# Performance work log

Hardware: AMD Instinct MI355X
Metric: run time of the kernel (lower is better)

Reference implementation:

```python
import jax, jax.numpy as jnp
import numpy as np

B, S, D, H, DH, L, FF = 1, 4096, 768, 12, 64, 12, 3072
V, P = 50265, 4098
BLK = 256          # block size for banded attention
W_ONE = 256        # one-sided window (attention_window=512)
EPS = 1e-5


def layernorm(x, g, b):
    mu = jnp.mean(x, axis=-1, keepdims=True)
    var = jnp.mean((x - mu) ** 2, axis=-1, keepdims=True)
    return (x - mu) * jax.lax.rsqrt(var + EPS) * g + b


def sliding_attn(q, k, v, mask):
    # q,k,v: [B,H,S,DH]; mask: [B,S] (1=keep). Band |i-j| <= W_ONE.
    nb = S // BLK
    scale = 1.0 / np.sqrt(DH)
    qb = (q * scale).reshape(B, H, nb, BLK, DH)
    kp = jnp.pad(k, ((0, 0), (0, 0), (BLK, BLK), (0, 0))).reshape(B, H, nb + 2, BLK, DH)
    vp = jnp.pad(v, ((0, 0), (0, 0), (BLK, BLK), (0, 0))).reshape(B, H, nb + 2, BLK, DH)
    # each query block attends to key blocks [b-1, b, b+1] -> 3*BLK keys
    kb = jnp.concatenate([kp[:, :, :-2], kp[:, :, 1:-1], kp[:, :, 2:]], axis=3)
    vb = jnp.concatenate([vp[:, :, :-2], vp[:, :, 1:-1], vp[:, :, 2:]], axis=3)
    scores = jnp.einsum('bhnqd,bhnkd->bhnqk', qb, kb)  # [B,H,nb,BLK,3BLK]
    p = jnp.arange(BLK)[:, None]
    o = jnp.arange(3 * BLK)[None, :]
    rel = o - BLK - p
    band = (rel >= -W_ONE) & (rel <= W_ONE)            # [BLK,3BLK]
    mp = jnp.pad(mask.astype(bool), ((0, 0), (BLK, BLK))).reshape(B, nb + 2, BLK)
    mb = jnp.concatenate([mp[:, :-2], mp[:, 1:-1], mp[:, 2:]], axis=2)  # [B,nb,3BLK]
    valid = band[None, None, None, :, :] & mb[:, None, :, None, :]
    scores = jnp.where(valid, scores, jnp.asarray(-1e9, scores.dtype))
    probs = jax.nn.softmax(scores, axis=-1)
    out = jnp.einsum('bhnqk,bhnkd->bhnqd', probs, vb)
    return out.reshape(B, H, S, DH)


def setup_inputs() -> dict:
    keys = iter(jax.random.split(jax.random.key(0), 64))
    rn = lambda shape, s=0.02: jax.random.normal(next(keys), shape, jnp.float32) * s
    inp = {
        'input_ids': jax.random.randint(next(keys), (B, S), 0, V, jnp.int32),
        'attention_mask': jnp.ones((B, S), jnp.int32),
        'emb_word': rn((V, D)), 'emb_pos': rn((P, D)), 'emb_type': rn((1, D)),
        'emb_ln_g': jnp.ones((D,)), 'emb_ln_b': jnp.zeros((D,)),
        'Wq': rn((L, D, D)), 'bq': jnp.zeros((L, D)),
        'Wk': rn((L, D, D)), 'bk': jnp.zeros((L, D)),
        'Wv': rn((L, D, D)), 'bv': jnp.zeros((L, D)),
        'Wo': rn((L, D, D)), 'bo': jnp.zeros((L, D)),
        'ln1_g': jnp.ones((L, D)), 'ln1_b': jnp.zeros((L, D)),
        'W1': rn((L, D, FF)), 'b1': jnp.zeros((L, FF)),
        'W2': rn((L, FF, D)), 'b2': jnp.zeros((L, D)),
        'ln2_g': jnp.ones((L, D)), 'ln2_b': jnp.zeros((L, D)),
        'cW1': rn((D, 512)), 'cb1': jnp.zeros((512,)),
        'cW2': rn((512, 5)), 'cb2': jnp.zeros((5,)),
        'dW1': rn((D, 512)), 'db1': jnp.zeros((512,)),
        'dW2': rn((512, 10)), 'db2': jnp.zeros((10,)),
    }
    return inp


def reference(input_ids, attention_mask, emb_word, emb_pos, emb_type, emb_ln_g, emb_ln_b,
              Wq, bq, Wk, bk, Wv, bv, Wo, bo, ln1_g, ln1_b, W1, b1, W2, b2, ln2_g, ln2_b,
              cW1, cb1, cW2, cb2, dW1, db1, dW2, db2):
    mask = attention_mask
    # RoBERTa-style position ids (pad_token_id=1 offset)
    pos_ids = jnp.cumsum(mask, axis=1) * mask + 1
    x = emb_word[input_ids] + emb_pos[pos_ids] + emb_type[0]
    x = layernorm(x, emb_ln_g, emb_ln_b)
    for i in range(L):
        q = (x @ Wq[i] + bq[i]).reshape(B, S, H, DH).transpose(0, 2, 1, 3)
        k = (x @ Wk[i] + bk[i]).reshape(B, S, H, DH).transpose(0, 2, 1, 3)
        v = (x @ Wv[i] + bv[i]).reshape(B, S, H, DH).transpose(0, 2, 1, 3)
        a = sliding_attn(q, k, v, mask).transpose(0, 2, 1, 3).reshape(B, S, D)
        x = layernorm(x + a @ Wo[i] + bo[i], ln1_g[i], ln1_b[i])
        h = jax.nn.gelu(x @ W1[i] + b1[i], approximate=False)
        x = layernorm(x + h @ W2[i] + b2[i], ln2_g[i], ln2_b[i])
    pooled = x[:, 0, :]
    century = jax.nn.relu(pooled @ cW1 + cb1) @ cW2 + cb2
    decade = jax.nn.relu(pooled @ dW1 + db1) @ dW2 + db2
    return (century, decade)
```

## Files before the change

### kernel.cpp

```cpp
#include <hip/hip_runtime.h>
#include <hip/hip_bf16.h>
#include <math.h>

typedef __bf16 bf16_t;
typedef __bf16 bf16x8 __attribute__((ext_vector_type(8)));
typedef __bf16 bf16x4 __attribute__((ext_vector_type(4)));
typedef float  f32x4  __attribute__((ext_vector_type(4)));
typedef short  s16x4  __attribute__((ext_vector_type(4)));

#define S_LEN 4096
#define DMODEL 768
#define NHEAD 12
#define NLAYER 12
#define FFDIM 3072

static __device__ inline f32x4 mfma16x16x16(bf16x4 a, bf16x4 b, f32x4 c) {
#if __has_builtin(__builtin_amdgcn_mfma_f32_16x16x16_bf16)
  return __builtin_amdgcn_mfma_f32_16x16x16_bf16(a, b, c, 0, 0, 0);
#else
  return __builtin_amdgcn_mfma_f32_16x16x16bf16_1k(
      __builtin_bit_cast(s16x4, a), __builtin_bit_cast(s16x4, b), c, 0, 0, 0);
#endif
}

__global__ __launch_bounds__(256) void posid_kernel(const int* __restrict__ m,
                                                    int* __restrict__ pids) {
  __shared__ int ps[256];
  int t = threadIdx.x;
  int base = t * 16;
  int loc[16], mv[16];
  int s = 0;
#pragma unroll
  for (int j = 0; j < 16; ++j) { mv[j] = m[base + j]; s += mv[j]; loc[j] = s; }
  ps[t] = s;
  __syncthreads();
  for (int off = 1; off < 256; off <<= 1) {
    int v = (t >= off) ? ps[t - off] : 0;
    __syncthreads();
    ps[t] += v;
    __syncthreads();
  }
  int pre = t ? ps[t - 1] : 0;
#pragma unroll
  for (int j = 0; j < 16; ++j) pids[base + j] = (pre + loc[j]) * mv[j] + 1;
}

__device__ inline float blk_sum(float v, float* sred) {
#pragma unroll
  for (int o = 32; o; o >>= 1) v += __shfl_down(v, o, 64);
  int w = threadIdx.x >> 6;
  __syncthreads();
  if ((threadIdx.x & 63) == 0) sred[w] = v;
  __syncthreads();
  return sred[0] + sred[1] + sred[2] + sred[3];
}

__global__ __launch_bounds__(256) void embed_kernel(
    const int* __restrict__ ids, const int* __restrict__ pids,
    const float* __restrict__ ew, const float* __restrict__ ep,
    const float* __restrict__ et, const float* __restrict__ g,
    const float* __restrict__ b, float* __restrict__ xf,
    bf16_t* __restrict__ xb) {
  __shared__ float sred[4];
  int s = blockIdx.x, t = threadIdx.x;
  long wb = (long)ids[s] * DMODEL;
  long pb = (long)pids[s] * DMODEL;
  float v[3];
#pragma unroll
  for (int j = 0; j < 3; ++j) {
    int d = t + j * 256;
    v[j] = ew[wb + d] + ep[pb + d] + et[d];
  }
  float mu = blk_sum(v[0] + v[1] + v[2], sred) * (1.0f / 768.0f);
  float ss = 0.f;
#pragma unroll
  for (int j = 0; j < 3; ++j) { v[j] -= mu; ss += v[j] * v[j]; }
  float rs = rsqrtf(blk_sum(ss, sred) * (1.0f / 768.0f) + 1e-5f);
#pragma unroll
  for (int j = 0; j < 3; ++j) {
    int d = t + j * 256;
    float o = v[j] * rs * g[d] + b[d];
    xf[(long)s * DMODEL + d] = o;
    xb[(long)s * DMODEL + d] = (bf16_t)o;
  }
}

__global__ __launch_bounds__(256) void ln_kernel(
    const float* __restrict__ in, const float* __restrict__ g,
    const float* __restrict__ b, float* __restrict__ xf,
    bf16_t* __restrict__ xb) {
  __shared__ float sred[4];
  int row = blockIdx.x, t = threadIdx.x;
  const float* r = in + (long)row * DMODEL;
  float v[3] = {r[t], r[t + 256], r[t + 512]};
  float mu = blk_sum(v[0] + v[1] + v[2], sred) * (1.0f / 768.0f);
  float ss = 0.f;
#pragma unroll
  for (int j = 0; j < 3; ++j) { v[j] -= mu; ss += v[j] * v[j]; }
  float rs = rsqrtf(blk_sum(ss, sred) * (1.0f / 768.0f) + 1e-5f);
#pragma unroll
  for (int j = 0; j < 3; ++j) {
    int d = t + j * 256;
    float o = v[j] * rs * g[d] + b[d];
    xf[(long)row * DMODEL + d] = o;
    xb[(long)row * DMODEL + d] = (bf16_t)o;
  }
}

__global__ __launch_bounds__(256) void trc_kernel(const float* __restrict__ src,
                                                  bf16_t* __restrict__ dst,
                                                  int R, int C, long srcStride,
                                                  long dstStride) {
  src += (long)blockIdx.z * srcStride;
  dst += (long)blockIdx.z * dstStride;
  __shared__ float tile[64][65];
  int r0 = blockIdx.y * 64, c0 = blockIdx.x * 64;
  int t = threadIdx.x;
  int tr = t >> 4;
  int tc = (t & 15) * 4;
#pragma unroll
  for (int j = 0; j < 4; ++j) {
    int row = tr + j * 16;
    float4 v = *(const float4*)(src + (long)(r0 + row) * C + c0 + tc);
    tile[row][tc] = v.x; tile[row][tc + 1] = v.y;
    tile[row][tc + 2] = v.z; tile[row][tc + 3] = v.w;
  }
  __syncthreads();
#pragma unroll
  for (int j = 0; j < 4; ++j) {
    int row = tr + j * 16;
    bf16x4 v;
    v[0] = (bf16_t)tile[tc + 0][row]; v[1] = (bf16_t)tile[tc + 1][row];
    v[2] = (bf16_t)tile[tc + 2][row]; v[3] = (bf16_t)tile[tc + 3][row];
    *(bf16x4*)(dst + (long)(c0 + row) * R + r0 + tc) = v;
  }
}

__global__ __launch_bounds__(256) void tr_kernel(const bf16_t* __restrict__ src,
                                                 bf16_t* __restrict__ dst,
                                                 int R, int C) {
  __shared__ bf16_t tile[64][68];
  int r0 = blockIdx.y * 64, c0 = blockIdx.x * 64;
  int t = threadIdx.x;
  int tr = t >> 4;
  int tc = (t & 15) * 4;
#pragma unroll
  for (int j = 0; j < 4; ++j) {
    int row = tr + j * 16;
    bf16x4 v = *(const bf16x4*)(src + (long)(r0 + row) * C + c0 + tc);
    tile[row][tc] = v[0]; tile[row][tc + 1] = v[1];
    tile[row][tc + 2] = v[2]; tile[row][tc + 3] = v[3];
  }
  __syncthreads();
#pragma unroll
  for (int j = 0; j < 4; ++j) {
    int row = tr + j * 16;
    bf16x4 v;
    v[0] = tile[tc + 0][row]; v[1] = tile[tc + 1][row];
    v[2] = tile[tc + 2][row]; v[3] = tile[tc + 3][row];
    *(bf16x4*)(dst + (long)(c0 + row) * R + r0 + tc) = v;
  }
}

template <int EP>
__global__ __launch_bounds__(256) void gemm_kernel(
    const bf16_t* __restrict__ A, const bf16_t* __restrict__ Bt, long btStride,
    const float* b0, const float* b1, const float* b2,
    bf16_t* __restrict__ out, long outStride, const float* __restrict__ resf,
    float* __restrict__ tmp, int M, int N, int K) {
  int z = blockIdx.z;
  Bt += (long)z * btStride;
  const float* bias = (z == 0) ? b0 : (z == 1 ? b1 : b2);
  out += (long)z * outStride;

  __shared__ __align__(16) bf16_t As[128 * 64];
  __shared__ __align__(16) bf16_t Bs[128 * 64];

  int tid = threadIdx.x;
  int lane = tid & 63;
  int wave = tid >> 6;
  int wm = (wave >> 1) * 64;
  int wn = (wave & 1) * 64;
  int l15 = lane & 15;
  int g4 = lane >> 4;
  int m0 = blockIdx.y * 128;
  int n0 = blockIdx.x * 128;

  f32x4 acc[4][4] = {};

  for (int kt = 0; kt < K; kt += 64) {
    bf16x8 avr[4], bvr[4];
#pragma unroll
    for (int c = 0; c < 4; ++c) {
      int L = c * 256 + tid;
      int gg = L >> 7, row = L & 127;
      avr[c] = *(const bf16x8*)(A + (long)(m0 + row) * K + kt + gg * 8);
      bvr[c] = *(const bf16x8*)(Bt + (long)(n0 + row) * K + kt + gg * 8);
    }
    __syncthreads();
#pragma unroll
    for (int c = 0; c < 4; ++c) {
      int L = c * 256 + tid;
      *(bf16x8*)(As + L * 8) = avr[c];
      *(bf16x8*)(Bs + L * 8) = bvr[c];
    }
    __syncthreads();
#pragma unroll
    for (int ks = 0; ks < 2; ++ks) {
      bf16x8 af[4], bfr[4];
#pragma unroll
      for (int mt = 0; mt < 4; ++mt)
        af[mt] = *(const bf16x8*)(As + (((ks * 4 + g4) * 128) + wm + mt * 16 + l15) * 8);
#pragma unroll
      for (int nt = 0; nt < 4; ++nt)
        bfr[nt] = *(const bf16x8*)(Bs + (((ks * 4 + g4) * 128) + wn + nt * 16 + l15) * 8);
#pragma unroll
      for (int mt = 0; mt < 4; ++mt)
#pragma unroll
        for (int nt = 0; nt < 4; ++nt)
          acc[mt][nt] = __builtin_amdgcn_mfma_f32_16x16x32_bf16(
              af[mt], bfr[nt], acc[mt][nt], 0, 0, 0);
    }
  }

#pragma unroll
  for (int mt = 0; mt < 4; ++mt)
#pragma unroll
    for (int nt = 0; nt < 4; ++nt) {
      int col = n0 + wn + nt * 16 + l15;
      float bval = bias[col];
#pragma unroll
      for (int r = 0; r < 4; ++r) {
        int row = m0 + wm + mt * 16 + g4 * 4 + r;
        float v = acc[mt][nt][r] + bval;
        if (EP == 0) {
          out[(long)row * N + col] = (bf16_t)v;
        } else if (EP == 1) {
          float ge = 0.5f * v * (1.0f + erff(v * 0.70710678118654752f));
          out[(long)row * N + col] = (bf16_t)ge;
        } else {
          tmp[(long)row * N + col] = v + resf[(long)row * N + col];
        }
      }
    }
}

#define NEGM 30000.0f
__global__ __launch_bounds__(64) void attn_kernel(
    const bf16_t* __restrict__ q, const bf16_t* __restrict__ k,
    const bf16_t* __restrict__ vt, bf16_t* __restrict__ outb) {
  int qt = blockIdx.x * 64;
  int hcol = blockIdx.y * 64;
  int lane = threadIdx.x;
  int l15 = lane & 15, g4 = lane >> 4;
  __shared__ __align__(16) float sbuf[64];

  bf16x8 qf[4][2];
#pragma unroll
  for (int nt = 0; nt < 4; ++nt)
#pragma unroll
    for (int ks = 0; ks < 2; ++ks) {
      bf16x8 t = *(const bf16x8*)(q + (long)(qt + nt * 16 + l15) * DMODEL +
                                  hcol + ks * 32 + g4 * 8);
#pragma unroll
      for (int i = 0; i < 8; ++i) t[i] = (bf16_t)((float)t[i] * 0.125f);
      qf[nt][ks] = t;
    }

  f32x4 o[4][4] = {};
  float mS[4], lS[4];
#pragma unroll
  for (int nt = 0; nt < 4; ++nt) { mS[nt] = -NEGM; lS[nt] = 0.f; }

  int kstart = qt - 256; if (kstart < 0) kstart = 0;
  int kend = qt + 320; if (kend > S_LEN) kend = S_LEN;

  for (int kb = kstart; kb < kend; kb += 64) {
    bf16x8 kf[4][2];
#pragma unroll
    for (int kt = 0; kt < 4; ++kt)
#pragma unroll
      for (int ks = 0; ks < 2; ++ks)
        kf[kt][ks] = *(const bf16x8*)(k + (long)(kb + kt * 16 + l15) * DMODEL +
                                      hcol + ks * 32 + g4 * 8);
    f32x4 st[4][4] = {};
#pragma unroll
    for (int kt = 0; kt < 4; ++kt)
#pragma unroll
      for (int nt = 0; nt < 4; ++nt) {
        st[kt][nt] = __builtin_amdgcn_mfma_f32_16x16x32_bf16(
            kf[kt][0], qf[nt][0], st[kt][nt], 0, 0, 0);
        st[kt][nt] = __builtin_amdgcn_mfma_f32_16x16x32_bf16(
            kf[kt][1], qf[nt][1], st[kt][nt], 0, 0, 0);
      }
    float alpha[4];
#pragma unroll
    for (int nt = 0; nt < 4; ++nt) {
      int qg = qt + nt * 16 + l15;
      float mx = -NEGM;
#pragma unroll
      for (int kt = 0; kt < 4; ++kt)
#pragma unroll
        for (int r = 0; r < 4; ++r) {
          int kg = kb + kt * 16 + g4 * 4 + r;
          bool valid = (kg >= qg - 256) && (kg <= qg + 256);
          float s = valid ? st[kt][nt][r] : -NEGM;
          st[kt][nt][r] = s;
          mx = fmaxf(mx, s);
        }
      mx = fmaxf(mx, __shfl_xor(mx, 16, 64));
      mx = fmaxf(mx, __shfl_xor(mx, 32, 64));
      float mnew = fmaxf(mS[nt], mx);
      alpha[nt] = exp2f((mS[nt] - mnew) * 1.44269504088896f);
      float ls = 0.f;
#pragma unroll
      for (int kt = 0; kt < 4; ++kt)
#pragma unroll
        for (int r = 0; r < 4; ++r) {
          float p = exp2f((st[kt][nt][r] - mnew) * 1.44269504088896f);
          st[kt][nt][r] = p;
          ls += p;
        }
      ls += __shfl_xor(ls, 16, 64);
      ls += __shfl_xor(ls, 32, 64);
      lS[nt] = lS[nt] * alpha[nt] + ls;
      mS[nt] = mnew;
    }
    if (g4 == 0) {
#pragma unroll
      for (int nt = 0; nt < 4; ++nt) sbuf[nt * 16 + l15] = alpha[nt];
    }
    __syncthreads();
    f32x4 av[4];
#pragma unroll
    for (int qmt = 0; qmt < 4; ++qmt)
      av[qmt] = *(const f32x4*)(sbuf + qmt * 16 + g4 * 4);
#pragma unroll
    for (int qmt = 0; qmt < 4; ++qmt)
#pragma unroll
      for (int dt = 0; dt < 4; ++dt)
#pragma unroll
        for (int r = 0; r < 4; ++r) o[qmt][dt][r] *= av[qmt][r];
#pragma unroll
    for (int kt = 0; kt < 4; ++kt) {
      bf16x4 pa[4];
#pragma unroll
      for (int qmt = 0; qmt < 4; ++qmt)
#pragma unroll
        for (int i = 0; i < 4; ++i) pa[qmt][i] = (bf16_t)st[kt][qmt][i];
      bf16x4 vf[4];
#pragma unroll
      for (int dt = 0; dt < 4; ++dt)
        vf[dt] = *(const bf16x4*)(vt + (long)(hcol + dt * 16 + l15) * S_LEN +
                                  kb + kt * 16 + g4 * 4);
#pragma unroll
      for (int qmt = 0; qmt < 4; ++qmt)
#pragma unroll
        for (int dt = 0; dt < 4; ++dt)
          o[qmt][dt] = mfma16x16x16(pa[qmt], vf[dt], o[qmt][dt]);
    }
    __syncthreads();
  }
  if (g4 == 0) {
#pragma unroll
    for (int nt = 0; nt < 4; ++nt) sbuf[nt * 16 + l15] = lS[nt];
  }
  __syncthreads();
  f32x4 lv[4];
#pragma unroll
  for (int qmt = 0; qmt < 4; ++qmt)
    lv[qmt] = *(const f32x4*)(sbuf + qmt * 16 + g4 * 4);
#pragma unroll
  for (int qmt = 0; qmt < 4; ++qmt)
#pragma unroll
    for (int dt = 0; dt < 4; ++dt)
#pragma unroll
      for (int r = 0; r < 4; ++r)
        outb[(long)(qt + qmt * 16 + g4 * 4 + r) * DMODEL + hcol + dt * 16 +
             l15] = (bf16_t)(o[qmt][dt][r] / lv[qmt][r]);
}

__global__ __launch_bounds__(256) void cls_kernel(
    const float* __restrict__ xf, const float* cW1, const float* cb1,
    const float* cW2, const float* cb2, const float* dW1,
    const float* db1, const float* dW2, const float* db2,
    float* __restrict__ out) {
  __shared__ float pooled[768];
  __shared__ float hbuf[512];
  int t = threadIdx.x;
  bool dec = (blockIdx.x == 1);
  const float* W1 = dec ? dW1 : cW1;
  const float* B1 = dec ? db1 : cb1;
  const float* W2 = dec ? dW2 : cW2;
  const float* B2 = dec ? db2 : cb2;
  int nout = dec ? 10 : 5;
  float* op = out + (dec ? 5 : 0);
#pragma unroll
  for (int j = 0; j < 3; ++j) pooled[t + j * 256] = xf[t + j * 256];
  __syncthreads();
  for (int n = t; n < 512; n += 256) {
    float a = B1[n];
    for (int k2 = 0; k2 < 768; ++k2)
      a += pooled[k2] * W1[(long)k2 * 512 + n];
    hbuf[n] = fmaxf(a, 0.f);
  }
  __syncthreads();
  if (t < nout) {
    float a = B2[t];
    for (int i = 0; i < 512; ++i) a += hbuf[i] * W2[i * nout + t];
    op[t] = a;
  }
}

extern "C" void kernel_launch(void* const* d_in, const int* in_sizes, int n_in,
                              void* d_out, int out_size, void* d_ws,
                              size_t ws_size, hipStream_t stream) {
  const int* ids = (const int*)d_in[0];
  const int* amask = (const int*)d_in[1];
  const float* emb_word = (const float*)d_in[2];
  const float* emb_pos = (const float*)d_in[3];
  const float* emb_type = (const float*)d_in[4];
  const float* emb_g = (const float*)d_in[5];
  const float* emb_b = (const float*)d_in[6];
  const float* Wq = (const float*)d_in[7];
  const float* bq = (const float*)d_in[8];
  const float* Wk = (const float*)d_in[9];
  const float* bk = (const float*)d_in[10];
  const float* Wv = (const float*)d_in[11];
  const float* bv = (const float*)d_in[12];
  const float* Wo = (const float*)d_in[13];
  const float* bo = (const float*)d_in[14];
  const float* ln1g = (const float*)d_in[15];
  const float* ln1b = (const float*)d_in[16];
  const float* W1 = (const float*)d_in[17];
  const float* b1 = (const float*)d_in[18];
  const float* W2 = (const float*)d_in[19];
  const float* b2 = (const float*)d_in[20];
  const float* ln2g = (const float*)d_in[21];
  const float* ln2b = (const float*)d_in[22];
  const float* cW1 = (const float*)d_in[23];
  const float* cb1 = (const float*)d_in[24];
  const float* cW2 = (const float*)d_in[25];
  const float* cb2 = (const float*)d_in[26];
  const float* dW1 = (const float*)d_in[27];
  const float* db1 = (const float*)d_in[28];
  const float* dW2 = (const float*)d_in[29];
  const float* db2 = (const float*)d_in[30];
  float* outp = (float*)d_out;

  const size_t SD = (size_t)S_LEN * DMODEL;
  const size_t DD = (size_t)DMODEL * DMODEL;
  const size_t DF = (size_t)DMODEL * FFDIM;
  const size_t SF = (size_t)S_LEN * FFDIM;

  char* p = (char*)d_ws;
  auto carve = [&](size_t bytes) {
    char* r = p;
    p += (bytes + 255) & ~(size_t)255;
    return (void*)r;
  };

  size_t actsBytes = SD * 2 + SD * 4 + 3 * SD * 2 + SD * 2 + SD * 2 + SF * 2 +
                     SD * 4 + S_LEN * 4 + 16 * 256;
  size_t fullW = (36 * DD + 12 * DD + 24 * DF) * 2 + 16 * 256;
  bool full = ws_size >= actsBytes + fullW;

  bf16_t *qkvt, *wot, *w1t, *w2t;
  if (full) {
    qkvt = (bf16_t*)carve(36 * DD * 2);
    wot = (bf16_t*)carve(12 * DD * 2);
    w1t = (bf16_t*)carve(12 * DF * 2);
    w2t = (bf16_t*)carve(12 * DF * 2);
  } else {
    qkvt = (bf16_t*)carve(3 * DD * 2);
    wot = (bf16_t*)carve(DD * 2);
    w1t = (bf16_t*)carve(DF * 2);
    w2t = (bf16_t*)carve(DF * 2);
  }
  bf16_t* xb = (bf16_t*)carve(SD * 2);
  float* xf = (float*)carve(SD * 4);
  bf16_t* qkv = (bf16_t*)carve(3 * SD * 2);
  bf16_t* vt = (bf16_t*)carve(SD * 2);
  bf16_t* attnb = (bf16_t*)carve(SD * 2);
  bf16_t* hbuf = (bf16_t*)carve(SF * 2);
  float* tmp = (float*)carve(SD * 4);
  int* pids = (int*)carve(S_LEN * 4);

  posid_kernel<<<1, 256, 0, stream>>>(amask, pids);
  embed_kernel<<<S_LEN, 256, 0, stream>>>(ids, pids, emb_word, emb_pos,
                                          emb_type, emb_g, emb_b, xf, xb);

  if (full) {
    trc_kernel<<<dim3(12, 12, 12), 256, 0, stream>>>(Wq, qkvt, 768, 768, DD, 3 * DD);
    trc_kernel<<<dim3(12, 12, 12), 256, 0, stream>>>(Wk, qkvt + DD, 768, 768, DD, 3 * DD);
    trc_kernel<<<dim3(12, 12, 12), 256, 0, stream>>>(Wv, qkvt + 2 * DD, 768, 768, DD, 3 * DD);
    trc_kernel<<<dim3(12, 12, 12), 256, 0, stream>>>(Wo, wot, 768, 768, DD, DD);
    trc_kernel<<<dim3(48, 12, 12), 256, 0, stream>>>(W1, w1t, 768, 3072, DF, DF);
    trc_kernel<<<dim3(12, 48, 12), 256, 0, stream>>>(W2, w2t, 3072, 768, DF, DF);
  }

  for (int i = 0; i < NLAYER; ++i) {
    const bf16_t *qkvt_i, *wot_i, *w1t_i, *w2t_i;
    if (full) {
      qkvt_i = qkvt + (size_t)i * 3 * DD;
      wot_i = wot + (size_t)i * DD;
      w1t_i = w1t + (size_t)i * DF;
      w2t_i = w2t + (size_t)i * DF;
    } else {
      trc_kernel<<<dim3(12, 12, 1), 256, 0, stream>>>(Wq + (size_t)i * DD, qkvt, 768, 768, 0, 0);
      trc_kernel<<<dim3(12, 12, 1), 256, 0, stream>>>(Wk + (size_t)i * DD, qkvt + DD, 768, 768, 0, 0);
      trc_kernel<<<dim3(12, 12, 1), 256, 0, stream>>>(Wv + (size_t)i * DD, qkvt + 2 * DD, 768, 768, 0, 0);
      trc_kernel<<<dim3(12, 12, 1), 256, 0, stream>>>(Wo + (size_t)i * DD, wot, 768, 768, 0, 0);
      trc_kernel<<<dim3(48, 12, 1), 256, 0, stream>>>(W1 + (size_t)i * DF, w1t, 768, 3072, 0, 0);
      trc_kernel<<<dim3(12, 48, 1), 256, 0, stream>>>(W2 + (size_t)i * DF, w2t, 3072, 768, 0, 0);
      qkvt_i = qkvt; wot_i = wot; w1t_i = w1t; w2t_i = w2t;
    }
    gemm_kernel<0><<<dim3(6, 32, 3), 256, 0, stream>>>(
        xb, qkvt_i, (long)DD, bq + i * 768, bk + i * 768, bv + i * 768, qkv,
        (long)SD, nullptr, nullptr, S_LEN, 768, 768);
    tr_kernel<<<dim3(12, 64, 1), 256, 0, stream>>>(qkv + 2 * SD, vt, 4096, 768);
    attn_kernel<<<dim3(64, 12), 64, 0, stream>>>(qkv, qkv + SD, vt, attnb);
    gemm_kernel<2><<<dim3(6, 32, 1), 256, 0, stream>>>(
        attnb, wot_i, 0, bo + i * 768, nullptr, nullptr, nullptr, 0, xf, tmp,
        S_LEN, 768, 768);
    ln_kernel<<<S_LEN, 256, 0, stream>>>(tmp, ln1g + i * 768, ln1b + i * 768, xf, xb);
    gemm_kernel<1><<<dim3(24, 32, 1), 256, 0, stream>>>(
        xb, w1t_i, 0, b1 + (size_t)i * FFDIM, nullptr, nullptr, hbuf, 0,
        nullptr, nullptr, S_LEN, FFDIM, 768);
    gemm_kernel<2><<<dim3(6, 32, 1), 256, 0, stream>>>(
        hbuf, w2t_i, 0, b2 + i * 768, nullptr, nullptr, nullptr, 0, xf, tmp,
        S_LEN, 768, FFDIM);
    ln_kernel<<<S_LEN, 256, 0, stream>>>(tmp, ln2g + i * 768, ln2b + i * 768, xf, xb);
  }
  cls_kernel<<<2, 256, 0, stream>>>(xf, cW1, cb1, cW2, cb2, dW1, db1, dW2, db2, outp);
}
```

Before: 4.114 ms.

## Double-buffer GEMM tiles with direct global-to-LDS async loads

The GEMM main loop now stages A and B tiles straight into shared memory with global_load_lds, skipping the register round trip. Two LDS buffers let the next K tile load while MFMAs run on the current one, synchronised with manual vmcnt waits and barriers. This aims to hide global memory latency and remove a sync per iteration. In exchange it doubles LDS use to 64KB per block, which can lower occupancy, and correctness now depends on the hand-written waitcnt counts.

```diff
diff --git a/kernel.cpp b/kernel.cpp
--- a/kernel.cpp
+++ b/kernel.cpp
@@ -21,6 +21,12 @@
   return __builtin_amdgcn_mfma_f32_16x16x16bf16_1k(
       __builtin_bit_cast(s16x4, a), __builtin_bit_cast(s16x4, b), c, 0, 0, 0);
 #endif
+}
+
+static __device__ inline void gload_lds16(const void* g, void* l) {
+  __builtin_amdgcn_global_load_lds(
+      (const __attribute__((address_space(1))) void*)g,
+      (__attribute__((address_space(3))) void*)l, 16, 0, 0);
 }
 
 __global__ __launch_bounds__(256) void posid_kernel(const int* __restrict__ m,
@@ -173,8 +179,8 @@
   const float* bias = (z == 0) ? b0 : (z == 1 ? b1 : b2);
   out += (long)z * outStride;
 
-  __shared__ __align__(16) bf16_t As[128 * 64];
-  __shared__ __align__(16) bf16_t Bs[128 * 64];
+  __shared__ __align__(16) bf16_t As[2][128 * 64];
+  __shared__ __align__(16) bf16_t Bs[2][128 * 64];
 
   int tid = threadIdx.x;
   int lane = tid & 63;
@@ -188,32 +194,40 @@
 
   f32x4 acc[4][4] = {};
 
-  for (int kt = 0; kt < K; kt += 64) {
-    bf16x8 avr[4], bvr[4];
+  auto stage = [&](int buf, int kt) {
 #pragma unroll
     for (int c = 0; c < 4; ++c) {
-      int L = c * 256 + tid;
-      int gg = L >> 7, row = L & 127;
-      avr[c] = *(const bf16x8*)(A + (long)(m0 + row) * K + kt + gg * 8);
-      bvr[c] = *(const bf16x8*)(Bt + (long)(n0 + row) * K + kt + gg * 8);
-    }
-    __syncthreads();
-#pragma unroll
-    for (int c = 0; c < 4; ++c) {
-      int L = c * 256 + tid;
-      *(bf16x8*)(As + L * 8) = avr[c];
-      *(bf16x8*)(Bs + L * 8) = bvr[c];
-    }
-    __syncthreads();
+      int L0 = c * 256 + wave * 64;
+      int row = (L0 & 127) + lane;
+      int gg = L0 >> 7;
+      gload_lds16(A + (long)(m0 + row) * K + kt + gg * 8, As[buf] + L0 * 8);
+      gload_lds16(Bt + (long)(n0 + row) * K + kt + gg * 8, Bs[buf] + L0 * 8);
+    }
+  };
+
+  int nk = K >> 6;
+  stage(0, 0);
+  int buf = 0;
+  for (int it = 0; it < nk; ++it) {
+    if (it + 1 < nk) {
+      stage(buf ^ 1, (it + 1) << 6);
+      asm volatile("s_waitcnt vmcnt(8)" ::: "memory");
+    } else {
+      asm volatile("s_waitcnt vmcnt(0)" ::: "memory");
+    }
+    __builtin_amdgcn_s_barrier();
+    __builtin_amdgcn_sched_barrier(0);
 #pragma unroll
     for (int ks = 0; ks < 2; ++ks) {
       bf16x8 af[4], bfr[4];
 #pragma unroll
       for (int mt = 0; mt < 4; ++mt)
-        af[mt] = *(const bf16x8*)(As + (((ks * 4 + g4) * 128) + wm + mt * 16 + l15) * 8);
+        af[mt] = *(const bf16x8*)(As[buf] +
+                                  (((ks * 4 + g4) * 128) + wm + mt * 16 + l15) * 8);
 #pragma unroll
       for (int nt = 0; nt < 4; ++nt)
-        bfr[nt] = *(const bf16x8*)(Bs + (((ks * 4 + g4) * 128) + wn + nt * 16 + l15) * 8);
+        bfr[nt] = *(const bf16x8*)(Bs[buf] +
+                                   (((ks * 4 + g4) * 128) + wn + nt * 16 + l15) * 8);
 #pragma unroll
       for (int mt = 0; mt < 4; ++mt)
 #pragma unroll
@@ -221,6 +235,9 @@
           acc[mt][nt] = __builtin_amdgcn_mfma_f32_16x16x32_bf16(
               af[mt], bfr[nt], acc[mt][nt], 0, 0, 0);
     }
+    __builtin_amdgcn_sched_barrier(0);
+    __builtin_amdgcn_s_barrier();
+    buf ^= 1;
   }
 
 #pragma unroll
```

Result: slower. 4.252 ms (+3.4%).

## Split-K the N=768 GEMMs with fused reduce+LayerNorm, direct-to-LDS loads, block swizzle

Applied to the files above, without the earlier changes.

The output-projection and FFN-down GEMMs, which launch only 192 workgroups, are split along K into 2 and 4 slices. Each slice writes fp32 partials, and a new kernel sums them with the bias and residual before applying LayerNorm. All GEMMs now load tiles with global_load_lds straight into shared memory instead of staging through registers, and they remap workgroup ids with a swizzle for cache locality. This trades extra partial-sum memory traffic and an added barrier per K step for more parallelism and less register staging.

```diff
diff --git a/kernel.cpp b/kernel.cpp
--- a/kernel.cpp
+++ b/kernel.cpp
@@ -21,6 +21,12 @@
   return __builtin_amdgcn_mfma_f32_16x16x16bf16_1k(
       __builtin_bit_cast(s16x4, a), __builtin_bit_cast(s16x4, b), c, 0, 0, 0);
 #endif
+}
+
+static __device__ inline void gload_lds16(const void* g, void* l) {
+  __builtin_amdgcn_global_load_lds(
+      (const __attribute__((address_space(1))) void*)g,
+      (__attribute__((address_space(3))) void*)l, 16, 0, 0);
 }
 
 __global__ __launch_bounds__(256) void posid_kernel(const int* __restrict__ m,
@@ -107,6 +113,36 @@
   }
 }
 
+__global__ __launch_bounds__(256) void lnred_kernel(
+    const float* __restrict__ pt, int ns, const float* __restrict__ gb,
+    const float* __restrict__ g, const float* __restrict__ b,
+    float* __restrict__ xf, bf16_t* __restrict__ xb) {
+  __shared__ float sred[4];
+  const long MN = (long)S_LEN * DMODEL;
+  int row = blockIdx.x, t = threadIdx.x;
+  long rb = (long)row * DMODEL;
+  float v[3];
+#pragma unroll
+  for (int j = 0; j < 3; ++j) {
+    int d = t + j * 256;
+    float a = gb[d] + xf[rb + d];
+    for (int z = 0; z < ns; ++z) a += pt[(long)z * MN + rb + d];
+    v[j] = a;
+  }
+  float mu = blk_sum(v[0] + v[1] + v[2], sred) * (1.0f / 768.0f);
+  float ss = 0.f;
+#pragma unroll
+  for (int j = 0; j < 3; ++j) { v[j] -= mu; ss += v[j] * v[j]; }
+  float rs = rsqrtf(blk_sum(ss, sred) * (1.0f / 768.0f) + 1e-5f);
+#pragma unroll
+  for (int j = 0; j < 3; ++j) {
+    int d = t + j * 256;
+    float o = v[j] * rs * g[d] + b[d];
+    xf[rb + d] = o;
+    xb[rb + d] = (bf16_t)o;
+  }
+}
+
 __global__ __launch_bounds__(256) void trc_kernel(const float* __restrict__ src,
                                                   bf16_t* __restrict__ dst,
                                                   int R, int C, long srcStride,
@@ -167,14 +203,23 @@
     const bf16_t* __restrict__ A, const bf16_t* __restrict__ Bt, long btStride,
     const float* b0, const float* b1, const float* b2,
     bf16_t* __restrict__ out, long outStride, const float* __restrict__ resf,
-    float* __restrict__ tmp, int M, int N, int K) {
+    float* __restrict__ tmp, int M, int N, int K, int kc) {
   int z = blockIdx.z;
-  Bt += (long)z * btStride;
-  const float* bias = (z == 0) ? b0 : (z == 1 ? b1 : b2);
-  out += (long)z * outStride;
-
-  __shared__ __align__(16) bf16_t As[128 * 64];
-  __shared__ __align__(16) bf16_t Bs[128 * 64];
+  const float* bias = nullptr;
+  int kBeg = 0;
+  if constexpr (EP == 3) {
+    kBeg = z * kc;
+  } else {
+    Bt += (long)z * btStride;
+    bias = (z == 0) ? b0 : (z == 1 ? b1 : b2);
+    out += (long)z * outStride;
+  }
+
+  int nwg = gridDim.x * gridDim.y;
+  int bid = blockIdx.y * gridDim.x + blockIdx.x;
+  int swz = (bid & 7) * (nwg >> 3) + (bid >> 3);
+  int bx = swz % gridDim.x;
+  int by = swz / gridDim.x;
 
   int tid = threadIdx.x;
   int lane = tid & 63;
@@ -183,26 +228,22 @@
   int wn = (wave & 1) * 64;
   int l15 = lane & 15;
   int g4 = lane >> 4;
-  int m0 = blockIdx.y * 128;
-  int n0 = blockIdx.x * 128;
+  int m0 = by * 128;
+  int n0 = bx * 128;
 
   f32x4 acc[4][4] = {};
 
-  for (int kt = 0; kt < K; kt += 64) {
-    bf16x8 avr[4], bvr[4];
+  __shared__ __align__(16) bf16_t As[128 * 64];
+  __shared__ __align__(16) bf16_t Bs[128 * 64];
+
+  for (int kt = kBeg; kt < kBeg + kc; kt += 64) {
 #pragma unroll
     for (int c = 0; c < 4; ++c) {
-      int L = c * 256 + tid;
-      int gg = L >> 7, row = L & 127;
-      avr[c] = *(const bf16x8*)(A + (long)(m0 + row) * K + kt + gg * 8);
-      bvr[c] = *(const bf16x8*)(Bt + (long)(n0 + row) * K + kt + gg * 8);
-    }
-    __syncthreads();
-#pragma unroll
-    for (int c = 0; c < 4; ++c) {
-      int L = c * 256 + tid;
-      *(bf16x8*)(As + L * 8) = avr[c];
-      *(bf16x8*)(Bs + L * 8) = bvr[c];
+      int L0 = c * 256 + wave * 64;
+      int row = (L0 & 127) + lane;
+      int gg = L0 >> 7;
+      gload_lds16(A + (long)(m0 + row) * K + kt + gg * 8, As + L0 * 8);
+      gload_lds16(Bt + (long)(n0 + row) * K + kt + gg * 8, Bs + L0 * 8);
     }
     __syncthreads();
 #pragma unroll
@@ -221,6 +262,7 @@
           acc[mt][nt] = __builtin_amdgcn_mfma_f32_16x16x32_bf16(
               af[mt], bfr[nt], acc[mt][nt], 0, 0, 0);
     }
+    __syncthreads();
   }
 
 #pragma unroll
@@ -228,7 +270,7 @@
 #pragma unroll
     for (int nt = 0; nt < 4; ++nt) {
       int col = n0 + wn + nt * 16 + l15;
-      float bval = bias[col];
+      float bval = (EP == 3) ? 0.f : bias[col];
 #pragma unroll
       for (int r = 0; r < 4; ++r) {
         int row = m0 + wm + mt * 16 + g4 * 4 + r;
@@ -238,8 +280,10 @@
         } else if (EP == 1) {
           float ge = 0.5f * v * (1.0f + erff(v * 0.70710678118654752f));
           out[(long)row * N + col] = (bf16_t)ge;
+        } else if (EP == 2) {
+          tmp[(long)row * N + col] = v + resf[(long)row * N + col];
         } else {
-          tmp[(long)row * N + col] = v + resf[(long)row * N + col];
+          tmp[(long)z * ((long)M * N) + (long)row * N + col] = v;
         }
       }
     }
@@ -485,6 +529,8 @@
   bf16_t* hbuf = (bf16_t*)carve(SF * 2);
   float* tmp = (float*)carve(SD * 4);
   int* pids = (int*)carve(S_LEN * 4);
+  float* ptmp = (float*)carve(4 * SD * 4);
+  bool haveSplit = ((size_t)(p - (char*)d_ws) <= ws_size);
 
   posid_kernel<<<1, 256, 0, stream>>>(amask, pids);
   embed_kernel<<<S_LEN, 256, 0, stream>>>(ids, pids, emb_word, emb_pos,
@@ -517,20 +563,40 @@
     }
     gemm_kernel<0><<<dim3(6, 32, 3), 256, 0, stream>>>(
         xb, qkvt_i, (long)DD, bq + i * 768, bk + i * 768, bv + i * 768, qkv,
-        (long)SD, nullptr, nullptr, S_LEN, 768, 768);
+        (long)SD, nullptr, nullptr, S_LEN, 768, 768, 768);
     tr_kernel<<<dim3(12, 64, 1), 256, 0, stream>>>(qkv + 2 * SD, vt, 4096, 768);
     attn_kernel<<<dim3(64, 12), 64, 0, stream>>>(qkv, qkv + SD, vt, attnb);
-    gemm_kernel<2><<<dim3(6, 32, 1), 256, 0, stream>>>(
-        attnb, wot_i, 0, bo + i * 768, nullptr, nullptr, nullptr, 0, xf, tmp,
-        S_LEN, 768, 768);
-    ln_kernel<<<S_LEN, 256, 0, stream>>>(tmp, ln1g + i * 768, ln1b + i * 768, xf, xb);
+    if (haveSplit) {
+      gemm_kernel<3><<<dim3(6, 32, 2), 256, 0, stream>>>(
+          attnb, wot_i, 0, nullptr, nullptr, nullptr, nullptr, 0, nullptr,
+          ptmp, S_LEN, 768, 768, 384);
+      lnred_kernel<<<S_LEN, 256, 0, stream>>>(ptmp, 2, bo + i * 768,
+                                              ln1g + i * 768, ln1b + i * 768,
+                                              xf, xb);
+    } else {
+      gemm_kernel<2><<<dim3(6, 32, 1), 256, 0, stream>>>(
+          attnb, wot_i, 0, bo + i * 768, nullptr, nullptr, nullptr, 0, xf, tmp,
+          S_LEN, 768, 768, 768);
+      ln_kernel<<<S_LEN, 256, 0, stream>>>(tmp, ln1g + i * 768, ln1b + i * 768,
+                                           xf, xb);
+    }
     gemm_kernel<1><<<dim3(24, 32, 1), 256, 0, stream>>>(
         xb, w1t_i, 0, b1 + (size_t)i * FFDIM, nullptr, nullptr, hbuf, 0,
-        nullptr, nullptr, S_LEN, FFDIM, 768);
-    gemm_kernel<2><<<dim3(6, 32, 1), 256, 0, stream>>>(
-        hbuf, w2t_i, 0, b2 + i * 768, nullptr, nullptr, nullptr, 0, xf, tmp,
-        S_LEN, 768, FFDIM);
-    ln_kernel<<<S_LEN, 256, 0, stream>>>(tmp, ln2g + i * 768, ln2b + i * 768, xf, xb);
+        nullptr, nullptr, S_LEN, FFDIM, 768, 768);
+    if (haveSplit) {
+      gemm_kernel<3><<<dim3(6, 32, 4), 256, 0, stream>>>(
+          hbuf, w2t_i, 0, nullptr, nullptr, nullptr, nullptr, 0, nullptr,
+          ptmp, S_LEN, 768, 3072, 768);
+      lnred_kernel<<<S_LEN, 256, 0, stream>>>(ptmp, 4, b2 + i * 768,
+                                              ln2g + i * 768, ln2b + i * 768,
+                                              xf, xb);
+    } else {
+      gemm_kernel<2><<<dim3(6, 32, 1), 256, 0, stream>>>(
+          hbuf, w2t_i, 0, b2 + i * 768, nullptr, nullptr, nullptr, 0, xf, tmp,
+          S_LEN, 768, 3072, 3072);
+      ln_kernel<<<S_LEN, 256, 0, stream>>>(tmp, ln2g + i * 768, ln2b + i * 768,
+                                           xf, xb);
+    }
   }
   cls_kernel<<<2, 256, 0, stream>>>(xf, cW1, cb1, cW2, cb2, dW1, db1, dW2, db2, outp);
 }
```

Measured after the change: 3.748 ms. -8.9%, faster.
